# Kernel tuning notes

Hardware: AMD Instinct MI355X
Metric: run time of the kernel (lower is better)

Reference implementation:

```python
import jax, jax.numpy as jnp
import numpy as np

BATCH = 64
DIM_IN = 4096
DIM_OUT = 4096


def setup_inputs() -> dict:
    key = jax.random.key(0)
    kx, km, kt = jax.random.split(key, 3)
    x = jax.random.bernoulli(kx, 0.5, (BATCH, DIM_IN))                      # bool [B, dim_in]
    masks = jax.random.bernoulli(km, 0.5, (DIM_IN, DIM_OUT))                # bool [dim_in, dim_out]
    thresholds = jax.random.randint(kt, (DIM_OUT,), 0, DIM_IN, dtype=jnp.int32)  # int [dim_out]
    return {"x": x, "masks": masks, "thresholds": thresholds}


def reference(x, masks, thresholds):
    # sum_i XNOR(x_i, m_ij) = #(both true) + #(both false)
    #                       = dim_in - sum_i x_i - sum_i m_ij + 2 * (x @ m)
    # This reproduces the broadcast-XNOR + reduce-sum math exactly without
    # materializing the [B, dim_in, dim_out] boolean tensor.
    xi = x.astype(jnp.int32)
    mi = masks.astype(jnp.int32)
    both_true = jnp.einsum('bi,io->bo', xi, mi)                             # int32 [B, dim_out]
    sums = DIM_IN - xi.sum(axis=1, keepdims=True) - mi.sum(axis=0, keepdims=True) + 2 * both_true
    return sums > thresholds[None, :]                                       # bool [B, dim_out]
```

## Files before the change

kernel.cpp:

```cpp
#include <hip/hip_runtime.h>
#include <stdint.h>

#define DIM_IN  4096
#define DIM_OUT 4096
#define BATCH   64

typedef unsigned long long u64;
typedef uint32_t u32;

__device__ __forceinline__ bool is_word_fmt(const u32* __restrict__ p) {
    bool words = true;
#pragma unroll
    for (int i = 0; i < 64; ++i) {
        u32 v = p[i];
        if (v > 1u && v != 0x3F800000u) words = false;
    }
    return words;
}

__global__ __launch_bounds__(256) void pack_kernel(
        const void* __restrict__ masks, const void* __restrict__ x,
        u64* __restrict__ mp, u64* __restrict__ xp) {
    if (blockIdx.y < 64) {
        const int w    = blockIdx.y;
        const int o0   = blockIdx.x * 1024 + threadIdx.x * 4;
        const int row0 = w * 64;
        const bool words = is_word_fmt((const u32*)masks);

        u32 lo[4] = {0u, 0u, 0u, 0u};
        u32 hi[4] = {0u, 0u, 0u, 0u};

        if (words) {
            const u32* pw = (const u32*)masks;
#pragma unroll 8
            for (int r = 0; r < 32; ++r) {
                const uint4 v = *reinterpret_cast<const uint4*>(
                    pw + (size_t)(row0 + r) * DIM_OUT + o0);
                lo[0] |= (u32)(v.x != 0u) << r;
                lo[1] |= (u32)(v.y != 0u) << r;
                lo[2] |= (u32)(v.z != 0u) << r;
                lo[3] |= (u32)(v.w != 0u) << r;
            }
#pragma unroll 8
            for (int r = 0; r < 32; ++r) {
                const uint4 v = *reinterpret_cast<const uint4*>(
                    pw + (size_t)(row0 + 32 + r) * DIM_OUT + o0);
                hi[0] |= (u32)(v.x != 0u) << r;
                hi[1] |= (u32)(v.y != 0u) << r;
                hi[2] |= (u32)(v.z != 0u) << r;
                hi[3] |= (u32)(v.w != 0u) << r;
            }
        } else {
            const u32* pb = (const u32*)masks;
            u32 s[8];
#pragma unroll
            for (int j = 0; j < 8; ++j) {
                u32 sl = 0u;
#pragma unroll
                for (int rr = 0; rr < 8; ++rr) {
                    u32 v = pb[((size_t)(row0 + j * 8 + rr) * DIM_OUT + o0) >> 2];
                    sl |= (v & 0x01010101u) << rr;
                }
                s[j] = sl;
            }
#pragma unroll
            for (int c = 0; c < 4; ++c) {
                const int sh = 8 * c;
                lo[c] = ((s[0] >> sh) & 0xFFu)
                      | (((s[1] >> sh) & 0xFFu) << 8)
                      | (((s[2] >> sh) & 0xFFu) << 16)
                      | (((s[3] >> sh) & 0xFFu) << 24);
                hi[c] = ((s[4] >> sh) & 0xFFu)
                      | (((s[5] >> sh) & 0xFFu) << 8)
                      | (((s[6] >> sh) & 0xFFu) << 16)
                      | (((s[7] >> sh) & 0xFFu) << 24);
            }
        }

        u64* dst = mp + (size_t)w * DIM_OUT + o0;
#pragma unroll
        for (int c = 0; c < 4; ++c)
            dst[c] = (u64)lo[c] | ((u64)hi[c] << 32);
    } else {
        const bool words = is_word_fmt((const u32*)x);
        const int bxid = (blockIdx.y - 64) * 4 + blockIdx.x;
        const int wave = bxid * 4 + (threadIdx.x >> 6);
        const int lane = threadIdx.x & 63;
        const int base = wave * 64;

#pragma unroll 16
        for (int k = 0; k < 64; ++k) {
            const int idx = base + k;
            const size_t e = (size_t)idx * 64 + lane;
            bool pred;
            if (words) pred = ((const u32*)x)[e] != 0u;
            else       pred = ((const uint8_t*)x)[e] != 0u;
            const u64 m = __ballot(pred);
            if (lane == 0) xp[idx] = m;
        }
    }
}

__global__ __launch_bounds__(256) void bnn_kernel(
        const u64* __restrict__ mp, const u64* __restrict__ xp,
        const int* __restrict__ thr, int* __restrict__ out) {
    const int o  = blockIdx.x * 256 + threadIdx.x;
    const int b0 = blockIdx.y * 4;

    const u64* __restrict__ x0 = xp + (size_t)(b0 + 0) * 64;
    const u64* __restrict__ x1 = xp + (size_t)(b0 + 1) * 64;
    const u64* __restrict__ x2 = xp + (size_t)(b0 + 2) * 64;
    const u64* __restrict__ x3 = xp + (size_t)(b0 + 3) * 64;

    int a0 = 0, a1 = 0, a2 = 0, a3 = 0;
#pragma unroll 16
    for (int w = 0; w < 64; ++w) {
        const u64 mw = mp[(size_t)w * DIM_OUT + o];
        a0 += __popcll(x0[w] ^ mw);
        a1 += __popcll(x1[w] ^ mw);
        a2 += __popcll(x2[w] ^ mw);
        a3 += __popcll(x3[w] ^ mw);
    }

    const int t = thr[o];
    out[(size_t)(b0 + 0) * DIM_OUT + o] = (DIM_IN - a0) > t ? 1 : 0;
    out[(size_t)(b0 + 1) * DIM_OUT + o] = (DIM_IN - a1) > t ? 1 : 0;
    out[(size_t)(b0 + 2) * DIM_OUT + o] = (DIM_IN - a2) > t ? 1 : 0;
    out[(size_t)(b0 + 3) * DIM_OUT + o] = (DIM_IN - a3) > t ? 1 : 0;
}

extern "C" void kernel_launch(void* const* d_in, const int* in_sizes, int n_in,
                              void* d_out, int out_size, void* d_ws, size_t ws_size,
                              hipStream_t stream) {
    const void* x     = d_in[0];
    const void* masks = d_in[1];
    const int*  thr   = (const int*)d_in[2];
    int* out = (int*)d_out;

    u64* mp = (u64*)d_ws;
    u64* xp = (u64*)((char*)d_ws + (size_t)64 * DIM_OUT * 8);

    pack_kernel<<<dim3(4, 68), dim3(256), 0, stream>>>(masks, x, mp, xp);
    bnn_kernel<<<dim3(16, 16), dim3(256), 0, stream>>>(mp, xp, thr, out);
}
```

Before: 40.58 us.

## Repartition mask packing to one column per thread across more blocks

The mask packing kernel moves from 256 blocks, where each thread handles 4 columns with uint4 loads, to 1024 blocks, where each thread packs a single column using 64 independent row loads issued in batches of 16. The goal is more parallelism and more memory requests in flight, so the GPU is better filled during the bandwidth-bound packing stage. The byte-format path now reads bytes directly rather than 32-bit words with bit shuffling, which makes each load narrower. The format detection check is cut from 64 probe words to 8, which makes misdetection more likely on unusual inputs.

```diff
diff --git a/kernel.cpp b/kernel.cpp
--- a/kernel.cpp
+++ b/kernel.cpp
@@ -11,7 +11,7 @@
 __device__ __forceinline__ bool is_word_fmt(const u32* __restrict__ p) {
     bool words = true;
 #pragma unroll
-    for (int i = 0; i < 64; ++i) {
+    for (int i = 0; i < 8; ++i) {
         u32 v = p[i];
         if (v > 1u && v != 0x3F800000u) words = false;
     }
@@ -21,69 +21,44 @@
 __global__ __launch_bounds__(256) void pack_kernel(
         const void* __restrict__ masks, const void* __restrict__ x,
         u64* __restrict__ mp, u64* __restrict__ xp) {
-    if (blockIdx.y < 64) {
-        const int w    = blockIdx.y;
-        const int o0   = blockIdx.x * 1024 + threadIdx.x * 4;
+    const int bid = blockIdx.x;
+    if (bid < 1024) {
+        const bool words = is_word_fmt((const u32*)masks);
+        const int wid = bid * 4 + (threadIdx.x >> 6);
+        const int w   = wid >> 6;
+        const int o   = ((wid & 63) << 6) + (threadIdx.x & 63);
         const int row0 = w * 64;
-        const bool words = is_word_fmt((const u32*)masks);
 
-        u32 lo[4] = {0u, 0u, 0u, 0u};
-        u32 hi[4] = {0u, 0u, 0u, 0u};
-
+        u64 bits = 0;
         if (words) {
-            const u32* pw = (const u32*)masks;
-#pragma unroll 8
-            for (int r = 0; r < 32; ++r) {
-                const uint4 v = *reinterpret_cast<const uint4*>(
-                    pw + (size_t)(row0 + r) * DIM_OUT + o0);
-                lo[0] |= (u32)(v.x != 0u) << r;
-                lo[1] |= (u32)(v.y != 0u) << r;
-                lo[2] |= (u32)(v.z != 0u) << r;
-                lo[3] |= (u32)(v.w != 0u) << r;
-            }
-#pragma unroll 8
-            for (int r = 0; r < 32; ++r) {
-                const uint4 v = *reinterpret_cast<const uint4*>(
-                    pw + (size_t)(row0 + 32 + r) * DIM_OUT + o0);
-                hi[0] |= (u32)(v.x != 0u) << r;
-                hi[1] |= (u32)(v.y != 0u) << r;
-                hi[2] |= (u32)(v.z != 0u) << r;
-                hi[3] |= (u32)(v.w != 0u) << r;
+            const u32* pw = (const u32*)masks + (size_t)row0 * DIM_OUT + o;
+#pragma unroll
+            for (int rb = 0; rb < 4; ++rb) {
+                u32 v[16];
+#pragma unroll
+                for (int r = 0; r < 16; ++r)
+                    v[r] = pw[(size_t)(rb * 16 + r) * DIM_OUT];
+#pragma unroll
+                for (int r = 0; r < 16; ++r)
+                    bits |= (u64)(v[r] != 0u) << (rb * 16 + r);
             }
         } else {
-            const u32* pb = (const u32*)masks;
-            u32 s[8];
+            const uint8_t* pb = (const uint8_t*)masks + (size_t)row0 * DIM_OUT + o;
 #pragma unroll
-            for (int j = 0; j < 8; ++j) {
-                u32 sl = 0u;
+            for (int rb = 0; rb < 4; ++rb) {
+                uint8_t v[16];
 #pragma unroll
-                for (int rr = 0; rr < 8; ++rr) {
-                    u32 v = pb[((size_t)(row0 + j * 8 + rr) * DIM_OUT + o0) >> 2];
-                    sl |= (v & 0x01010101u) << rr;
-                }
-                s[j] = sl;
-            }
+                for (int r = 0; r < 16; ++r)
+                    v[r] = pb[(size_t)(rb * 16 + r) * DIM_OUT];
 #pragma unroll
-            for (int c = 0; c < 4; ++c) {
-                const int sh = 8 * c;
-                lo[c] = ((s[0] >> sh) & 0xFFu)
-                      | (((s[1] >> sh) & 0xFFu) << 8)
-                      | (((s[2] >> sh) & 0xFFu) << 16)
-                      | (((s[3] >> sh) & 0xFFu) << 24);
-                hi[c] = ((s[4] >> sh) & 0xFFu)
-                      | (((s[5] >> sh) & 0xFFu) << 8)
-                      | (((s[6] >> sh) & 0xFFu) << 16)
-                      | (((s[7] >> sh) & 0xFFu) << 24);
+                for (int r = 0; r < 16; ++r)
+                    bits |= (u64)(v[r] != 0u) << (rb * 16 + r);
             }
         }
-
-        u64* dst = mp + (size_t)w * DIM_OUT + o0;
-#pragma unroll
-        for (int c = 0; c < 4; ++c)
-            dst[c] = (u64)lo[c] | ((u64)hi[c] << 32);
+        mp[(size_t)w * DIM_OUT + o] = bits;
     } else {
         const bool words = is_word_fmt((const u32*)x);
-        const int bxid = (blockIdx.y - 64) * 4 + blockIdx.x;
+        const int bxid = bid - 1024;
         const int wave = bxid * 4 + (threadIdx.x >> 6);
         const int lane = threadIdx.x & 63;
         const int base = wave * 64;
@@ -140,6 +115,6 @@
     u64* mp = (u64*)d_ws;
     u64* xp = (u64*)((char*)d_ws + (size_t)64 * DIM_OUT * 8);
 
-    pack_kernel<<<dim3(4, 68), dim3(256), 0, stream>>>(masks, x, mp, xp);
+    pack_kernel<<<dim3(1040), dim3(256), 0, stream>>>(masks, x, mp, xp);
     bnn_kernel<<<dim3(16, 16), dim3(256), 0, stream>>>(mp, xp, thr, out);
 }
```

New measurement: 42.41 us. 1.05x slower.
